# Optimization experiments

Hardware: AMD Instinct MI355X
Metric: run time of the kernel (lower is better)

The kernel has to match this reference:

```python
import jax, jax.numpy as jnp
import numpy as np


def setup_inputs() -> dict:
    key = jax.random.key(0)
    k1, k2, k3, k4 = jax.random.split(key, 4)
    B, C, H, W = 4, 256, 48, 48
    scale = 1.0 / np.sqrt(C)  # conv-like init scale
    x = jax.random.normal(k1, (B, C, H, W), dtype=jnp.float32)
    wq = jax.random.normal(k2, (C, C), dtype=jnp.float32) * scale
    wk = jax.random.normal(k3, (C, C), dtype=jnp.float32) * scale
    wv = jax.random.normal(k4, (C, C), dtype=jnp.float32) * scale
    return {"x": x, "wq": wq, "wk": wk, "wv": wv}


def reference(x, wq, wk, wv):
    B, C, H, W = x.shape
    num_heads = 8
    d_k = C // num_heads
    N = H * W

    # 1x1 convs (bias=False) are channel-mixing matmuls: [out_c, in_c]
    def proj(w):
        y = jnp.einsum('oc,bchw->bohw', w, x)
        # view(B, heads, d_k, H*W)
        return y.reshape(B, num_heads, d_k, N)

    q = proj(wq)  # [B, h, d_k, N]
    k = proj(wk)
    v = proj(wv)

    # scores = q^T k / sqrt(d_k) -> [B, h, N, N]
    scores = jnp.einsum('bhdn,bhdm->bhnm', q, k) / jnp.sqrt(jnp.asarray(d_k, x.dtype))
    attn = jax.nn.softmax(scores, axis=-1)
    # out = attn @ v^T -> [B, h, N, d_k]
    out = jnp.einsum('bhnm,bhdm->bhnd', attn, v)
    # permute back to [B, h, d_k, N] then view(B, C, H, W)
    out = out.transpose(0, 1, 3, 2).reshape(B, C, H, W)
    return x + out
```

## Files before the change

kernel.cpp:

```cpp
#include <hip/hip_runtime.h>

constexpr int B  = 4;
constexpr int C  = 256;
constexpr int N  = 2304;
constexpr int NH = 8;
constexpr int DK = 32;

typedef short short8 __attribute__((ext_vector_type(8)));
typedef float f32x4  __attribute__((ext_vector_type(4)));

static __device__ __forceinline__ ushort f2bf(float f) {
    union { float f; unsigned u; } v; v.f = f;
    return (ushort)((v.u + 0x7FFFu + ((v.u >> 16) & 1u)) >> 16);
}
static __device__ __forceinline__ unsigned cvtpk(float lo, float hi) {
    unsigned r;
    asm("v_cvt_pk_bf16_f32 %0, %1, %2" : "=v"(r) : "v"(lo), "v"(hi));
    return r;
}

__global__ __launch_bounds__(256) void proj_kernel(
    const float* __restrict__ x,
    const float* __restrict__ wq,
    const float* __restrict__ wk,
    const float* __restrict__ wv,
    ushort* __restrict__ ws,
    int bfix, size_t matStride, size_t batchStride)
{
    const int tile = blockIdx.x;
    const int mat  = blockIdx.y;
    const int b    = (bfix >= 0) ? bfix : (int)blockIdx.z;
    const int n0 = (tile % (N / 64)) * 64;
    const int o0 = (tile / (N / 64)) * 64;

    const float* w = (mat == 0) ? wq : (mat == 1) ? wk : wv;
    ushort* out = ws + (size_t)mat * matStride + (size_t)b * batchStride;
    const float* xb = x + (size_t)b * C * N;

    __shared__ float xs[16][64];
    __shared__ float wt[64][17];

    const int tid = threadIdx.x;
    const int tx = tid & 15;
    const int ty = tid >> 4;

    float acc[4][4] = {};

    for (int k0 = 0; k0 < C; k0 += 16) {
        {
            const int kk  = tid >> 4;
            const int nn4 = tid & 15;
            float4 v = *reinterpret_cast<const float4*>(xb + (size_t)(k0 + kk) * N + n0 + nn4 * 4);
            *reinterpret_cast<float4*>(&xs[kk][nn4 * 4]) = v;
        }
        {
            const int oo = tid >> 2;
            const int k4 = tid & 3;
            float4 v = *reinterpret_cast<const float4*>(w + (size_t)(o0 + oo) * C + k0 + k4 * 4);
            wt[oo][k4 * 4 + 0] = v.x;
            wt[oo][k4 * 4 + 1] = v.y;
            wt[oo][k4 * 4 + 2] = v.z;
            wt[oo][k4 * 4 + 3] = v.w;
        }
        __syncthreads();

        #pragma unroll
        for (int kk = 0; kk < 16; ++kk) {
            float4 a = *reinterpret_cast<const float4*>(&xs[kk][tx * 4]);
            float av[4] = {a.x, a.y, a.z, a.w};
            float bv[4];
            #pragma unroll
            for (int jo = 0; jo < 4; ++jo) bv[jo] = wt[ty * 4 + jo][kk];
            #pragma unroll
            for (int jo = 0; jo < 4; ++jo)
                #pragma unroll
                for (int jn = 0; jn < 4; ++jn)
                    acc[jo][jn] = fmaf(bv[jo], av[jn], acc[jo][jn]);
        }
        __syncthreads();
    }

    const float sc = (mat == 0) ? 0.25503450535f : 1.0f;
    #pragma unroll
    for (int jn = 0; jn < 4; ++jn) {
        ushort4 wv4 = make_ushort4(f2bf(acc[0][jn] * sc), f2bf(acc[1][jn] * sc),
                                   f2bf(acc[2][jn] * sc), f2bf(acc[3][jn] * sc));
        *reinterpret_cast<ushort4*>(out + (size_t)(n0 + tx * 4 + jn) * C + o0 + ty * 4) = wv4;
    }
}

__global__ __launch_bounds__(128) void attn_kernel(
    const ushort* __restrict__ ws,
    const float* __restrict__ x,
    float* __restrict__ out,
    int bfix, size_t matStride, size_t batchStride, int ppx)
{
    __shared__ __align__(16) char smem[14336];
    ushort* Ks  = (ushort*)smem;
    ushort* Vt  = (ushort*)(smem + 5120);
    float*  Ost = (float*) smem;

    const int tid = threadIdx.x;
    const int wq  = tid >> 6;
    const int l   = tid & 63;
    const int lq  = l & 15;
    const int g   = l >> 4;

    ushort* Pl = (ushort*)(smem + 9728) + wq * 1152;

    const int gid  = blockIdx.x;
    const int xcd  = gid & 7;
    const int loc  = gid >> 3;
    const int pair = xcd * ppx + loc / 72;
    const int qt   = loc % 72;
    const int h    = pair & 7;
    const int b    = (bfix >= 0) ? bfix : (pair >> 3);
    const int n0   = qt * 32;

    const ushort* qb = ws + (size_t)b * batchStride;
    const ushort* kb = qb + matStride;
    const ushort* vb = qb + 2 * matStride;

    short8 qf = *reinterpret_cast<const short8*>(
        qb + (size_t)(n0 + wq * 16 + lq) * C + h * DK + 8 * g);

    f32x4 acc0 = {0.f, 0.f, 0.f, 0.f};
    f32x4 acc1 = {0.f, 0.f, 0.f, 0.f};
    float m = -1e30f, lsum = 0.f;

    const int kr = tid >> 2, kc = tid & 3;
    const int vp = tid & 31, vd = tid >> 5;

    short8  kreg0, kreg1;
    ushort4 va0, vc0, va1, vc1;

    #define LOAD_TILE(m0_)                                                          \
        {                                                                           \
            const int m0i = (m0_);                                                  \
            kreg0 = *reinterpret_cast<const short8*>(kb + (size_t)(m0i + kr) * C + h * DK + kc * 8);        \
            kreg1 = *reinterpret_cast<const short8*>(kb + (size_t)(m0i + 32 + kr) * C + h * DK + kc * 8);   \
            const ushort* v0 = vb + (size_t)(m0i + 2 * vp) * C + h * DK + vd * 4;   \
            va0 = *reinterpret_cast<const ushort4*>(v0);                            \
            vc0 = *reinterpret_cast<const ushort4*>(v0 + C);                        \
            va1 = *reinterpret_cast<const ushort4*>(v0 + 16);                       \
            vc1 = *reinterpret_cast<const ushort4*>(v0 + C + 16);                   \
        }

    LOAD_TILE(0);

    for (int t = 0; t < N / 64; ++t) {
        *reinterpret_cast<short8*>(Ks + kr * 40 + kc * 8) = kreg0;
        *reinterpret_cast<short8*>(Ks + (kr + 32) * 40 + kc * 8) = kreg1;
        {
            unsigned p0 = (unsigned)va0.x | ((unsigned)vc0.x << 16);
            unsigned p1 = (unsigned)va0.y | ((unsigned)vc0.y << 16);
            unsigned p2 = (unsigned)va0.z | ((unsigned)vc0.z << 16);
            unsigned p3 = (unsigned)va0.w | ((unsigned)vc0.w << 16);
            *reinterpret_cast<unsigned*>(Vt + (vd * 4 + 0) * 72 + 2 * vp) = p0;
            *reinterpret_cast<unsigned*>(Vt + (vd * 4 + 1) * 72 + 2 * vp) = p1;
            *reinterpret_cast<unsigned*>(Vt + (vd * 4 + 2) * 72 + 2 * vp) = p2;
            *reinterpret_cast<unsigned*>(Vt + (vd * 4 + 3) * 72 + 2 * vp) = p3;
            unsigned q0 = (unsigned)va1.x | ((unsigned)vc1.x << 16);
            unsigned q1 = (unsigned)va1.y | ((unsigned)vc1.y << 16);
            unsigned q2 = (unsigned)va1.z | ((unsigned)vc1.z << 16);
            unsigned q3 = (unsigned)va1.w | ((unsigned)vc1.w << 16);
            *reinterpret_cast<unsigned*>(Vt + (vd * 4 + 16) * 72 + 2 * vp) = q0;
            *reinterpret_cast<unsigned*>(Vt + (vd * 4 + 17) * 72 + 2 * vp) = q1;
            *reinterpret_cast<unsigned*>(Vt + (vd * 4 + 18) * 72 + 2 * vp) = q2;
            *reinterpret_cast<unsigned*>(Vt + (vd * 4 + 19) * 72 + 2 * vp) = q3;
        }
        __syncthreads();

        if (t < N / 64 - 1) LOAD_TILE((t + 1) * 64);

        f32x4 st[4];
        __builtin_amdgcn_s_setprio(1);
        #pragma unroll
        for (int u = 0; u < 4; ++u) {
            short8 kf = *reinterpret_cast<const short8*>(Ks + (lq + 16 * u) * 40 + 8 * g);
            f32x4 z = {0.f, 0.f, 0.f, 0.f};
            st[u] = __builtin_amdgcn_mfma_f32_16x16x32_bf16(kf, qf, z, 0, 0, 0);
        }
        __builtin_amdgcn_s_setprio(0);

        float mxl = st[0][0];
        #pragma unroll
        for (int u = 0; u < 4; ++u)
            #pragma unroll
            for (int r = 0; r < 4; ++r) mxl = fmaxf(mxl, st[u][r]);

        if (!__all(mxl <= m + 8.0f)) {
            float mx = fmaxf(mxl, __shfl_xor(mxl, 16));
            mx = fmaxf(mx, __shfl_xor(mx, 32));
            float nm = fmaxf(m, mx);
            float corr = exp2f(m - nm);
            m = nm;
            lsum *= corr;
            float cw0 = __shfl(corr, 4 * g + 0);
            float cw1 = __shfl(corr, 4 * g + 1);
            float cw2 = __shfl(corr, 4 * g + 2);
            float cw3 = __shfl(corr, 4 * g + 3);
            acc0[0] *= cw0; acc0[1] *= cw1; acc0[2] *= cw2; acc0[3] *= cw3;
            acc1[0] *= cw0; acc1[1] *= cw1; acc1[2] *= cw2; acc1[3] *= cw3;
        }

        float ps = 0.f;
        uint2 pw[4];
        #pragma unroll
        for (int u = 0; u < 4; ++u) {
            float p0 = exp2f(st[u][0] - m);
            float p1 = exp2f(st[u][1] - m);
            float p2 = exp2f(st[u][2] - m);
            float p3 = exp2f(st[u][3] - m);
            ps += (p0 + p1) + (p2 + p3);
            pw[u].x = cvtpk(p0, p1);
            pw[u].y = cvtpk(p2, p3);
        }
        lsum += ps;

        #pragma unroll
        for (int u = 0; u < 4; ++u)
            *reinterpret_cast<uint2*>(Pl + lq * 72 + 4 * g + 16 * u) = pw[u];

        short8 pf0 = *reinterpret_cast<const short8*>(Pl + lq * 72 + 8 * g);
        short8 pf1 = *reinterpret_cast<const short8*>(Pl + lq * 72 + 32 + 8 * g);
        __builtin_amdgcn_s_setprio(1);
        #pragma unroll
        for (int k2 = 0; k2 < 2; ++k2) {
            short8 pf = k2 ? pf1 : pf0;
            short8 vf0 = *reinterpret_cast<const short8*>(Vt + lq * 72 + 32 * k2 + 8 * g);
            short8 vf1 = *reinterpret_cast<const short8*>(Vt + (lq + 16) * 72 + 32 * k2 + 8 * g);
            acc0 = __builtin_amdgcn_mfma_f32_16x16x32_bf16(pf, vf0, acc0, 0, 0, 0);
            acc1 = __builtin_amdgcn_mfma_f32_16x16x32_bf16(pf, vf1, acc1, 0, 0, 0);
        }
        __builtin_amdgcn_s_setprio(0);
        __syncthreads();
    }

    lsum += __shfl_xor(lsum, 16);
    lsum += __shfl_xor(lsum, 32);
    const float iv = 1.0f / lsum;
    float iw0 = __shfl(iv, 4 * g + 0);
    float iw1 = __shfl(iv, 4 * g + 1);
    float iw2 = __shfl(iv, 4 * g + 2);
    float iw3 = __shfl(iv, 4 * g + 3);

    Ost[(lq +  0) * 36 + wq * 16 + 4 * g + 0] = acc0[0] * iw0;
    Ost[(lq +  0) * 36 + wq * 16 + 4 * g + 1] = acc0[1] * iw1;
    Ost[(lq +  0) * 36 + wq * 16 + 4 * g + 2] = acc0[2] * iw2;
    Ost[(lq +  0) * 36 + wq * 16 + 4 * g + 3] = acc0[3] * iw3;
    Ost[(lq + 16) * 36 + wq * 16 + 4 * g + 0] = acc1[0] * iw0;
    Ost[(lq + 16) * 36 + wq * 16 + 4 * g + 1] = acc1[1] * iw1;
    Ost[(lq + 16) * 36 + wq * 16 + 4 * g + 2] = acc1[2] * iw2;
    Ost[(lq + 16) * 36 + wq * 16 + 4 * g + 3] = acc1[3] * iw3;
    __syncthreads();

    {
        const int d  = tid >> 2;
        const int nn = (tid & 3) * 8;
        const size_t go = ((size_t)b * C + h * DK + d) * (size_t)N + n0 + nn;
        float4 o1 = *reinterpret_cast<float4*>(Ost + d * 36 + nn);
        float4 o2 = *reinterpret_cast<float4*>(Ost + d * 36 + nn + 4);
        float4 x1 = *reinterpret_cast<const float4*>(x + go);
        float4 x2 = *reinterpret_cast<const float4*>(x + go + 4);
        *reinterpret_cast<float4*>(out + go)     = make_float4(o1.x + x1.x, o1.y + x1.y, o1.z + x1.z, o1.w + x1.w);
        *reinterpret_cast<float4*>(out + go + 4) = make_float4(o2.x + x2.x, o2.y + x2.y, o2.z + x2.z, o2.w + x2.w);
    }
}

extern "C" void kernel_launch(void* const* d_in, const int* in_sizes, int n_in,
                              void* d_out, int out_size, void* d_ws, size_t ws_size,
                              hipStream_t stream) {
    const float* x  = (const float*)d_in[0];
    const float* wq = (const float*)d_in[1];
    const float* wk = (const float*)d_in[2];
    const float* wv = (const float*)d_in[3];
    float* out = (float*)d_out;
    ushort* ws = (ushort*)d_ws;

    const size_t NC = (size_t)N * C;
    const size_t needFull = 3 * (size_t)B * NC * sizeof(ushort);

    if (ws_size >= needFull) {
        proj_kernel<<<dim3((N / 64) * (C / 64), 3, B), 256, 0, stream>>>(
            x, wq, wk, wv, ws, -1, (size_t)B * NC, NC);
        attn_kernel<<<dim3(72 * NH * B), 128, 0, stream>>>(
            ws, x, out, -1, (size_t)B * NC, NC, 4);
    } else {
        for (int b = 0; b < B; ++b) {
            proj_kernel<<<dim3((N / 64) * (C / 64), 3, 1), 256, 0, stream>>>(
                x, wq, wk, wv, ws, b, NC, 0);
            attn_kernel<<<dim3(72 * NH), 128, 0, stream>>>(
                ws, x, out, b, NC, 0, 1);
        }
    }
}
```

Before: 229.6 us.

## Load K/V MFMA fragments directly from global, store V transposed

The projection kernel now writes V transposed ([C][N] layout) so the attention kernel can load V fragments straight from global memory. The attention kernel drops the shared-memory K/V staging and the two per-tile barriers, and instead register double-buffers per-lane K and V fragments across tiles. This removes LDS traffic and synchronisation, at the cost of more VGPRs and uncoalesced, redundant global loads, since each wave fetches the K/V data itself.

```diff
diff --git a/kernel.cpp b/kernel.cpp
--- a/kernel.cpp
+++ b/kernel.cpp
@@ -80,12 +80,21 @@
         __syncthreads();
     }
 
-    const float sc = (mat == 0) ? 0.25503450535f : 1.0f;
-    #pragma unroll
-    for (int jn = 0; jn < 4; ++jn) {
-        ushort4 wv4 = make_ushort4(f2bf(acc[0][jn] * sc), f2bf(acc[1][jn] * sc),
-                                   f2bf(acc[2][jn] * sc), f2bf(acc[3][jn] * sc));
-        *reinterpret_cast<ushort4*>(out + (size_t)(n0 + tx * 4 + jn) * C + o0 + ty * 4) = wv4;
+    if (mat == 2) {
+        #pragma unroll
+        for (int jo = 0; jo < 4; ++jo) {
+            ushort4 w4 = make_ushort4(f2bf(acc[jo][0]), f2bf(acc[jo][1]),
+                                      f2bf(acc[jo][2]), f2bf(acc[jo][3]));
+            *reinterpret_cast<ushort4*>(out + (size_t)(o0 + ty * 4 + jo) * N + n0 + tx * 4) = w4;
+        }
+    } else {
+        const float sc = (mat == 0) ? 0.25503450535f : 1.0f;
+        #pragma unroll
+        for (int jn = 0; jn < 4; ++jn) {
+            ushort4 w4 = make_ushort4(f2bf(acc[0][jn] * sc), f2bf(acc[1][jn] * sc),
+                                      f2bf(acc[2][jn] * sc), f2bf(acc[3][jn] * sc));
+            *reinterpret_cast<ushort4*>(out + (size_t)(n0 + tx * 4 + jn) * C + o0 + ty * 4) = w4;
+        }
     }
 }
 
@@ -95,10 +104,7 @@
     float* __restrict__ out,
     int bfix, size_t matStride, size_t batchStride, int ppx)
 {
-    __shared__ __align__(16) char smem[14336];
-    ushort* Ks  = (ushort*)smem;
-    ushort* Vt  = (ushort*)(smem + 5120);
-    float*  Ost = (float*) smem;
+    __shared__ __align__(16) char smem[9216];
 
     const int tid = threadIdx.x;
     const int wq  = tid >> 6;
@@ -106,7 +112,8 @@
     const int lq  = l & 15;
     const int g   = l >> 4;
 
-    ushort* Pl = (ushort*)(smem + 9728) + wq * 1152;
+    ushort* Pl = (ushort*)smem + wq * 1152;
+    float*  Ost = (float*)(smem + 4608);
 
     const int gid  = blockIdx.x;
     const int xcd  = gid & 7;
@@ -117,125 +124,112 @@
     const int b    = (bfix >= 0) ? bfix : (pair >> 3);
     const int n0   = qt * 32;
 
-    const ushort* qb = ws + (size_t)b * batchStride;
-    const ushort* kb = qb + matStride;
-    const ushort* vb = qb + 2 * matStride;
+    const ushort* qbh = ws + (size_t)b * batchStride + h * DK;
+    const ushort* kbh = ws + matStride + (size_t)b * batchStride + h * DK;
+    const ushort* vth = ws + 2 * matStride + (size_t)b * batchStride + (size_t)h * DK * N;
 
     short8 qf = *reinterpret_cast<const short8*>(
-        qb + (size_t)(n0 + wq * 16 + lq) * C + h * DK + 8 * g);
+        qbh + (size_t)(n0 + wq * 16 + lq) * C + 8 * g);
 
     f32x4 acc0 = {0.f, 0.f, 0.f, 0.f};
     f32x4 acc1 = {0.f, 0.f, 0.f, 0.f};
     float m = -1e30f, lsum = 0.f;
 
-    const int kr = tid >> 2, kc = tid & 3;
-    const int vp = tid & 31, vd = tid >> 5;
-
-    short8  kreg0, kreg1;
-    ushort4 va0, vc0, va1, vc1;
-
-    #define LOAD_TILE(m0_)                                                          \
-        {                                                                           \
-            const int m0i = (m0_);                                                  \
-            kreg0 = *reinterpret_cast<const short8*>(kb + (size_t)(m0i + kr) * C + h * DK + kc * 8);        \
-            kreg1 = *reinterpret_cast<const short8*>(kb + (size_t)(m0i + 32 + kr) * C + h * DK + kc * 8);   \
-            const ushort* v0 = vb + (size_t)(m0i + 2 * vp) * C + h * DK + vd * 4;   \
-            va0 = *reinterpret_cast<const ushort4*>(v0);                            \
-            vc0 = *reinterpret_cast<const ushort4*>(v0 + C);                        \
-            va1 = *reinterpret_cast<const ushort4*>(v0 + 16);                       \
-            vc1 = *reinterpret_cast<const ushort4*>(v0 + C + 16);                   \
-        }
-
-    LOAD_TILE(0);
-
-    for (int t = 0; t < N / 64; ++t) {
-        *reinterpret_cast<short8*>(Ks + kr * 40 + kc * 8) = kreg0;
-        *reinterpret_cast<short8*>(Ks + (kr + 32) * 40 + kc * 8) = kreg1;
-        {
-            unsigned p0 = (unsigned)va0.x | ((unsigned)vc0.x << 16);
-            unsigned p1 = (unsigned)va0.y | ((unsigned)vc0.y << 16);
-            unsigned p2 = (unsigned)va0.z | ((unsigned)vc0.z << 16);
-            unsigned p3 = (unsigned)va0.w | ((unsigned)vc0.w << 16);
-            *reinterpret_cast<unsigned*>(Vt + (vd * 4 + 0) * 72 + 2 * vp) = p0;
-            *reinterpret_cast<unsigned*>(Vt + (vd * 4 + 1) * 72 + 2 * vp) = p1;
-            *reinterpret_cast<unsigned*>(Vt + (vd * 4 + 2) * 72 + 2 * vp) = p2;
-            *reinterpret_cast<unsigned*>(Vt + (vd * 4 + 3) * 72 + 2 * vp) = p3;
-            unsigned q0 = (unsigned)va1.x | ((unsigned)vc1.x << 16);
-            unsigned q1 = (unsigned)va1.y | ((unsigned)vc1.y << 16);
-            unsigned q2 = (unsigned)va1.z | ((unsigned)vc1.z << 16);
-            unsigned q3 = (unsigned)va1.w | ((unsigned)vc1.w << 16);
-            *reinterpret_cast<unsigned*>(Vt + (vd * 4 + 16) * 72 + 2 * vp) = q0;
-            *reinterpret_cast<unsigned*>(Vt + (vd * 4 + 17) * 72 + 2 * vp) = q1;
-            *reinterpret_cast<unsigned*>(Vt + (vd * 4 + 18) * 72 + 2 * vp) = q2;
-            *reinterpret_cast<unsigned*>(Vt + (vd * 4 + 19) * 72 + 2 * vp) = q3;
-        }
-        __syncthreads();
-
-        if (t < N / 64 - 1) LOAD_TILE((t + 1) * 64);
-
-        f32x4 st[4];
-        __builtin_amdgcn_s_setprio(1);
-        #pragma unroll
-        for (int u = 0; u < 4; ++u) {
-            short8 kf = *reinterpret_cast<const short8*>(Ks + (lq + 16 * u) * 40 + 8 * g);
-            f32x4 z = {0.f, 0.f, 0.f, 0.f};
-            st[u] = __builtin_amdgcn_mfma_f32_16x16x32_bf16(kf, qf, z, 0, 0, 0);
-        }
-        __builtin_amdgcn_s_setprio(0);
-
-        float mxl = st[0][0];
-        #pragma unroll
-        for (int u = 0; u < 4; ++u)
-            #pragma unroll
-            for (int r = 0; r < 4; ++r) mxl = fmaxf(mxl, st[u][r]);
-
-        if (!__all(mxl <= m + 8.0f)) {
-            float mx = fmaxf(mxl, __shfl_xor(mxl, 16));
-            mx = fmaxf(mx, __shfl_xor(mx, 32));
-            float nm = fmaxf(m, mx);
-            float corr = exp2f(m - nm);
-            m = nm;
-            lsum *= corr;
-            float cw0 = __shfl(corr, 4 * g + 0);
-            float cw1 = __shfl(corr, 4 * g + 1);
-            float cw2 = __shfl(corr, 4 * g + 2);
-            float cw3 = __shfl(corr, 4 * g + 3);
-            acc0[0] *= cw0; acc0[1] *= cw1; acc0[2] *= cw2; acc0[3] *= cw3;
-            acc1[0] *= cw0; acc1[1] *= cw1; acc1[2] *= cw2; acc1[3] *= cw3;
-        }
-
-        float ps = 0.f;
-        uint2 pw[4];
-        #pragma unroll
-        for (int u = 0; u < 4; ++u) {
-            float p0 = exp2f(st[u][0] - m);
-            float p1 = exp2f(st[u][1] - m);
-            float p2 = exp2f(st[u][2] - m);
-            float p3 = exp2f(st[u][3] - m);
-            ps += (p0 + p1) + (p2 + p3);
-            pw[u].x = cvtpk(p0, p1);
-            pw[u].y = cvtpk(p2, p3);
-        }
-        lsum += ps;
-
-        #pragma unroll
-        for (int u = 0; u < 4; ++u)
-            *reinterpret_cast<uint2*>(Pl + lq * 72 + 4 * g + 16 * u) = pw[u];
-
-        short8 pf0 = *reinterpret_cast<const short8*>(Pl + lq * 72 + 8 * g);
-        short8 pf1 = *reinterpret_cast<const short8*>(Pl + lq * 72 + 32 + 8 * g);
-        __builtin_amdgcn_s_setprio(1);
-        #pragma unroll
-        for (int k2 = 0; k2 < 2; ++k2) {
-            short8 pf = k2 ? pf1 : pf0;
-            short8 vf0 = *reinterpret_cast<const short8*>(Vt + lq * 72 + 32 * k2 + 8 * g);
-            short8 vf1 = *reinterpret_cast<const short8*>(Vt + (lq + 16) * 72 + 32 * k2 + 8 * g);
-            acc0 = __builtin_amdgcn_mfma_f32_16x16x32_bf16(pf, vf0, acc0, 0, 0, 0);
-            acc1 = __builtin_amdgcn_mfma_f32_16x16x32_bf16(pf, vf1, acc1, 0, 0, 0);
-        }
-        __builtin_amdgcn_s_setprio(0);
-        __syncthreads();
-    }
+    #define LOADT(KA0,KA1,KA2,KA3,VA0,VA1,VA2,VA3,TT) {                         \
+        const ushort* kt_ = kbh + (size_t)(TT) * 64 * C;                        \
+        const ushort* vt_ = vth + (TT) * 64;                                    \
+        KA0 = *reinterpret_cast<const short8*>(kt_ + (lq     ) * C + 8 * g);    \
+        KA1 = *reinterpret_cast<const short8*>(kt_ + (lq + 16) * C + 8 * g);    \
+        KA2 = *reinterpret_cast<const short8*>(kt_ + (lq + 32) * C + 8 * g);    \
+        KA3 = *reinterpret_cast<const short8*>(kt_ + (lq + 48) * C + 8 * g);    \
+        VA0 = *reinterpret_cast<const short8*>(vt_ + (size_t)(lq     ) * N + 8 * g);      \
+        VA1 = *reinterpret_cast<const short8*>(vt_ + (size_t)(lq + 16) * N + 8 * g);      \
+        VA2 = *reinterpret_cast<const short8*>(vt_ + (size_t)(lq     ) * N + 8 * g + 32); \
+        VA3 = *reinterpret_cast<const short8*>(vt_ + (size_t)(lq + 16) * N + 8 * g + 32); \
+    }
+
+    #define COMPUTE(KA0,KA1,KA2,KA3,VA0,VA1,VA2,VA3) {                          \
+        f32x4 z = {0.f, 0.f, 0.f, 0.f};                                         \
+        f32x4 s0, s1, s2, s3;                                                   \
+        __builtin_amdgcn_s_setprio(1);                                          \
+        s0 = __builtin_amdgcn_mfma_f32_16x16x32_bf16(KA0, qf, z, 0, 0, 0);      \
+        s1 = __builtin_amdgcn_mfma_f32_16x16x32_bf16(KA1, qf, z, 0, 0, 0);      \
+        s2 = __builtin_amdgcn_mfma_f32_16x16x32_bf16(KA2, qf, z, 0, 0, 0);      \
+        s3 = __builtin_amdgcn_mfma_f32_16x16x32_bf16(KA3, qf, z, 0, 0, 0);      \
+        __builtin_amdgcn_s_setprio(0);                                          \
+        float mxl = s0[0];                                                      \
+        _Pragma("unroll") for (int r = 0; r < 4; ++r) {                         \
+            mxl = fmaxf(mxl, s0[r]); mxl = fmaxf(mxl, s1[r]);                   \
+            mxl = fmaxf(mxl, s2[r]); mxl = fmaxf(mxl, s3[r]);                   \
+        }                                                                       \
+        if (!__all(mxl <= m + 8.0f)) {                                          \
+            float mx = fmaxf(mxl, __shfl_xor(mxl, 16));                         \
+            mx = fmaxf(mx, __shfl_xor(mx, 32));                                 \
+            float nm = fmaxf(m, mx);                                            \
+            float corr = exp2f(m - nm);                                         \
+            m = nm; lsum *= corr;                                               \
+            float cw0 = __shfl(corr, 4 * g + 0);                                \
+            float cw1 = __shfl(corr, 4 * g + 1);                                \
+            float cw2 = __shfl(corr, 4 * g + 2);                                \
+            float cw3 = __shfl(corr, 4 * g + 3);                                \
+            acc0[0] *= cw0; acc0[1] *= cw1; acc0[2] *= cw2; acc0[3] *= cw3;     \
+            acc1[0] *= cw0; acc1[1] *= cw1; acc1[2] *= cw2; acc1[3] *= cw3;     \
+        }                                                                       \
+        float ps = 0.f;                                                         \
+        uint2 pw0, pw1, pw2, pw3;                                               \
+        {                                                                       \
+            float p0 = exp2f(s0[0] - m), p1 = exp2f(s0[1] - m);                 \
+            float p2 = exp2f(s0[2] - m), p3 = exp2f(s0[3] - m);                 \
+            ps += (p0 + p1) + (p2 + p3);                                        \
+            pw0.x = cvtpk(p0, p1); pw0.y = cvtpk(p2, p3);                       \
+        }                                                                       \
+        {                                                                       \
+            float p0 = exp2f(s1[0] - m), p1 = exp2f(s1[1] - m);                 \
+            float p2 = exp2f(s1[2] - m), p3 = exp2f(s1[3] - m);                 \
+            ps += (p0 + p1) + (p2 + p3);                                        \
+            pw1.x = cvtpk(p0, p1); pw1.y = cvtpk(p2, p3);                       \
+        }                                                                       \
+        {                                                                       \
+            float p0 = exp2f(s2[0] - m), p1 = exp2f(s2[1] - m);                 \
+            float p2 = exp2f(s2[2] - m), p3 = exp2f(s2[3] - m);                 \
+            ps += (p0 + p1) + (p2 + p3);                                        \
+            pw2.x = cvtpk(p0, p1); pw2.y = cvtpk(p2, p3);                       \
+        }                                                                       \
+        {                                                                       \
+            float p0 = exp2f(s3[0] - m), p1 = exp2f(s3[1] - m);                 \
+            float p2 = exp2f(s3[2] - m), p3 = exp2f(s3[3] - m);                 \
+            ps += (p0 + p1) + (p2 + p3);                                        \
+            pw3.x = cvtpk(p0, p1); pw3.y = cvtpk(p2, p3);                       \
+        }                                                                       \
+        lsum += ps;                                                             \
+        *reinterpret_cast<uint2*>(Pl + lq * 72 + 4 * g     ) = pw0;             \
+        *reinterpret_cast<uint2*>(Pl + lq * 72 + 4 * g + 16) = pw1;             \
+        *reinterpret_cast<uint2*>(Pl + lq * 72 + 4 * g + 32) = pw2;             \
+        *reinterpret_cast<uint2*>(Pl + lq * 72 + 4 * g + 48) = pw3;             \
+        short8 pf0 = *reinterpret_cast<const short8*>(Pl + lq * 72 + 8 * g);    \
+        short8 pf1 = *reinterpret_cast<const short8*>(Pl + lq * 72 + 32 + 8 * g); \
+        __builtin_amdgcn_s_setprio(1);                                          \
+        acc0 = __builtin_amdgcn_mfma_f32_16x16x32_bf16(pf0, VA0, acc0, 0, 0, 0); \
+        acc1 = __builtin_amdgcn_mfma_f32_16x16x32_bf16(pf0, VA1, acc1, 0, 0, 0); \
+        acc0 = __builtin_amdgcn_mfma_f32_16x16x32_bf16(pf1, VA2, acc0, 0, 0, 0); \
+        acc1 = __builtin_amdgcn_mfma_f32_16x16x32_bf16(pf1, VA3, acc1, 0, 0, 0); \
+        __builtin_amdgcn_s_setprio(0);                                          \
+    }
+
+    short8 kA0, kA1, kA2, kA3, vA0, vA1, vA2, vA3;
+    short8 kB0, kB1, kB2, kB3, vB0, vB1, vB2, vB3;
+
+    LOADT(kA0,kA1,kA2,kA3, vA0,vA1,vA2,vA3, 0);
+
+    for (int t = 0; t < N / 64; t += 2) {
+        LOADT(kB0,kB1,kB2,kB3, vB0,vB1,vB2,vB3, t + 1);
+        COMPUTE(kA0,kA1,kA2,kA3, vA0,vA1,vA2,vA3);
+        const int t2 = (t + 2 == N / 64) ? 0 : t + 2;
+        LOADT(kA0,kA1,kA2,kA3, vA0,vA1,vA2,vA3, t2);
+        COMPUTE(kB0,kB1,kB2,kB3, vB0,vB1,vB2,vB3);
+    }
+    #undef LOADT
+    #undef COMPUTE
 
     lsum += __shfl_xor(lsum, 16);
     lsum += __shfl_xor(lsum, 32);
```

After: 299.7 us. 1.31x slower.
